# Kernel tuning notes

Measured on AMD Instinct MI355X. Metric: run time of the kernel, lower is better.

Reference implementation:

```python
import jax, jax.numpy as jnp
import numpy as np

B, S, H = 32, 512, 768
N, E, P = 4096, 131072, 65536
HEADS1, C1 = 4, 128
HEADS2, C2 = 1, 64
NUM_REL, REL_HID = 6, 256
NER_HID, NER_LAB = 256, 9
LRELU_SLOPE = 0.2  # PyG GATConv default negative_slope
LN_EPS = 1e-5


def setup_inputs() -> dict:
    key = jax.random.key(0)
    ks = jax.random.split(key, 24)
    sc = 0.02
    inp = {
        'sequence_output': jax.random.normal(ks[0], (B, S, H), jnp.float32),
        'ent_start': jax.random.randint(ks[1], (N,), 0, S - 8),
        'ent_len': jax.random.randint(ks[2], (N,), 0, 8),
        'ent_batch': jax.random.randint(ks[3], (N,), 0, B),
        'edge_index': jax.random.randint(ks[4], (2, E), 0, N),
        'pair_idx': jax.random.randint(ks[5], (P, 2), 0, N),
        'W1': jax.random.normal(ks[6], (H, HEADS1 * C1), jnp.float32) * sc,
        'a_src1': jax.random.normal(ks[7], (HEADS1, C1), jnp.float32) * sc,
        'a_dst1': jax.random.normal(ks[8], (HEADS1, C1), jnp.float32) * sc,
        'b1': jnp.zeros((HEADS1 * C1,), jnp.float32),
        'W2': jax.random.normal(ks[9], (HEADS1 * C1, HEADS2 * C2), jnp.float32) * sc,
        'a_src2': jax.random.normal(ks[10], (HEADS2, C2), jnp.float32) * sc,
        'a_dst2': jax.random.normal(ks[11], (HEADS2, C2), jnp.float32) * sc,
        'b2': jnp.zeros((HEADS2 * C2,), jnp.float32),
        # 6 per-relation classifiers: Linear(128,256)+LN+ReLU+Linear(256,1)
        'relW1': jax.random.normal(ks[12], (NUM_REL, 2 * C2, REL_HID), jnp.float32) * sc,
        'relb1': jnp.zeros((NUM_REL, REL_HID), jnp.float32),
        'ln_g': jnp.ones((NUM_REL, REL_HID), jnp.float32),
        'ln_b': jnp.zeros((NUM_REL, REL_HID), jnp.float32),
        'relW2': jax.random.normal(ks[13], (NUM_REL, REL_HID, 1), jnp.float32) * sc,
        'relb2': jnp.zeros((NUM_REL, 1), jnp.float32),
        # NER head: Linear(768,256)+ReLU+Linear(256,9)
        'nerW1': jax.random.normal(ks[14], (H, NER_HID), jnp.float32) * sc,
        'nerb1': jnp.zeros((NER_HID,), jnp.float32),
        'nerW2': jax.random.normal(ks[15], (NER_HID, NER_LAB), jnp.float32) * sc,
        'nerb2': jnp.zeros((NER_LAB,), jnp.float32),
    }
    return inp


def _gat(x, src, dst, W, a_src, a_dst, b, heads, ch, n):
    # PyG GATConv: per-head linear, additive attention, softmax over incoming edges
    h = (x @ W).reshape(n, heads, ch)                      # [N,Hd,C]
    e_src = jnp.sum(h * a_src, axis=-1)                    # [N,Hd]
    e_dst = jnp.sum(h * a_dst, axis=-1)
    e = jax.nn.leaky_relu(e_src[src] + e_dst[dst], LRELU_SLOPE)  # [E,Hd]
    m = jax.ops.segment_max(e, dst, num_segments=n)
    ex = jnp.exp(e - m[dst])
    denom = jax.ops.segment_sum(ex, dst, num_segments=n)
    alpha = ex / denom[dst]                                # [E,Hd]
    out = jax.ops.segment_sum(alpha[:, :, None] * h[src], dst, num_segments=n)
    return out.reshape(n, heads * ch) + b


def reference(sequence_output, ent_start, ent_len, ent_batch, edge_index, pair_idx,
              W1, a_src1, a_dst1, b1, W2, a_src2, a_dst2, b2,
              relW1, relb1, ln_g, ln_b, relW2, relb2,
              nerW1, nerb1, nerW2, nerb2):
    n = ent_start.shape[0]
    # NER head on the full sequence
    ner_logits = jax.nn.relu(sequence_output @ nerW1 + nerb1) @ nerW2 + nerb2  # [B,S,9]
    # Entity-span mean pooling via exclusive prefix sums (inclusive span start..start+len)
    csum = jnp.cumsum(sequence_output, axis=1)
    csum = jnp.concatenate([jnp.zeros((B, 1, H), sequence_output.dtype), csum], axis=1)  # [B,S+1,H]
    ent_end = ent_start + ent_len
    span_sum = csum[ent_batch, ent_end + 1] - csum[ent_batch, ent_start]  # [N,H]
    x = span_sum / (ent_len + 1).astype(span_sum.dtype)[:, None]
    # add self loops (PyG GATConv default add_self_loops=True)
    loops = jnp.arange(n, dtype=edge_index.dtype)
    src = jnp.concatenate([edge_index[0], loops])
    dst = jnp.concatenate([edge_index[1], loops])
    x = _gat(x, src, dst, W1, a_src1, a_dst1, b1, HEADS1, C1, n)
    x = jax.nn.relu(x)  # dropout p=0.3 is identity in eval mode
    x = _gat(x, src, dst, W2, a_src2, a_dst2, b2, HEADS2, C2, n)  # [N,64]
    # Pair features: cat(x[e1], x[e2]) -> [P,128]
    pair_feat = jnp.concatenate([x[pair_idx[:, 0]], x[pair_idx[:, 1]]], axis=-1)
    # All 6 relation classifiers, vectorized over the relation dim
    hid = jnp.einsum('pf,rfk->rpk', pair_feat, relW1) + relb1[:, None, :]  # [6,P,256]
    mu = jnp.mean(hid, axis=-1, keepdims=True)
    var = jnp.mean(jnp.square(hid - mu), axis=-1, keepdims=True)
    hid = (hid - mu) * jax.lax.rsqrt(var + LN_EPS) * ln_g[:, None, :] + ln_b[:, None, :]
    hid = jax.nn.relu(hid)
    rel_logits = (jnp.einsum('rpk,rko->rpo', hid, relW2) + relb2[:, None, :])[..., 0]  # [6,P]
    return ner_logits, rel_logits
```

## Files before the change

kernel.cpp:

```cpp
#include <hip/hip_runtime.h>
#include <math.h>

#define LRELU 0.2f

constexpr int Bn = 32, Sn = 512, Hn = 768, Nn = 4096, En = 131072, Pn = 65536;
constexpr int ET = En + Nn;

typedef __attribute__((ext_vector_type(8))) short bf16x8;
typedef __attribute__((ext_vector_type(4))) float f32x4;

constexpr size_t OFF_X0  = 0;
constexpr size_t OFF_UV  = 0;
constexpr size_t OFF_H1  = 4194304;
constexpr size_t OFF_X1  = OFF_H1  + 2097152;
constexpr size_t OFF_H2  = OFF_X1  + 2097152;
constexpr size_t OFF_X2  = OFF_H2  + 262144;
constexpr size_t OFF_ES1 = OFF_X2  + 262144;
constexpr size_t OFF_ED1 = OFF_ES1 + 16384;
constexpr size_t OFF_ES2 = OFF_ED1 + 16384;
constexpr size_t OFF_ED2 = OFF_ES2 + 4096;
constexpr size_t OFF_ROW = OFF_ED2 + 4096;
constexpr size_t OFF_CUR = OFF_ROW + 4104;
constexpr size_t OFF_EDG = OFF_CUR + 4096;
constexpr size_t OFF_W1S = OFF_EDG + 135168;
constexpr size_t OFF_NW1S = OFF_W1S + 196608;

__device__ __forceinline__ short f2bf(float f) {
  union { float f; unsigned u; } x; x.f = f;
  unsigned r = x.u + 0x7fff + ((x.u >> 16) & 1);
  return (short)(r >> 16);
}
__device__ __forceinline__ float bf2f(short s) {
  union { unsigned u; float f; } x;
  x.u = ((unsigned)(unsigned short)s) << 16;
  return x.f;
}

__global__ __launch_bounds__(256) void span_pool_k(
    const float* __restrict__ seq, const int* __restrict__ est,
    const int* __restrict__ eln, const int* __restrict__ ebt,
    float* __restrict__ x0) {
  int idx = blockIdx.x * 256 + threadIdx.x;
  if (idx >= Nn * (Hn / 4)) return;
  int e = idx / (Hn / 4);
  int c = (idx % (Hn / 4)) * 4;
  int s0 = est[e], L = eln[e] + 1, b = ebt[e];
  const float* p = seq + ((size_t)b * Sn + s0) * Hn + c;
  float ax = 0, ay = 0, az = 0, aw = 0;
  for (int i = 0; i < L; ++i) {
    float4 v = *(const float4*)(p + (size_t)i * Hn);
    ax += v.x; ay += v.y; az += v.z; aw += v.w;
  }
  float inv = 1.0f / (float)L;
  float4 o; o.x = ax * inv; o.y = ay * inv; o.z = az * inv; o.w = aw * inv;
  *(float4*)&x0[(size_t)e * Hn + c] = o;
}

template <int EPI, int NTW, int KC>
__global__ __launch_bounds__(256) void mfma_gemm_k(
    const float* __restrict__ A, const short* __restrict__ Bswz,
    float* __restrict__ C, const float* __restrict__ bias,
    int M, int K, int N) {
  constexpr int RS = KC + 8;
  __shared__ short at[64 * RS];
  int t = threadIdx.x;
  size_t rowb = (size_t)blockIdx.x * 64;
  int colb = blockIdx.y * (64 * NTW);
  int w = t >> 6, lane = t & 63, quad = lane >> 4, id = lane & 15;
  f32x4 acc[4][NTW];
#pragma unroll
  for (int mt = 0; mt < 4; ++mt)
#pragma unroll
    for (int nt = 0; nt < NTW; ++nt) acc[mt][nt] = (f32x4){0.f, 0.f, 0.f, 0.f};

  for (int k0 = 0; k0 < K; k0 += KC) {
    constexpr int CH = 64 * KC / 8 / 256;
#pragma unroll
    for (int i = 0; i < CH; ++i) {
      int cid = t + i * 256;
      int p = cid / (KC / 8), o8 = (cid % (KC / 8)) * 8;
      const float* src = &A[(rowb + p) * (size_t)K + k0 + o8];
      float4 v0 = *(const float4*)src;
      float4 v1 = *(const float4*)(src + 4);
      bf16x8 bv;
      bv[0] = f2bf(v0.x); bv[1] = f2bf(v0.y); bv[2] = f2bf(v0.z); bv[3] = f2bf(v0.w);
      bv[4] = f2bf(v1.x); bv[5] = f2bf(v1.y); bv[6] = f2bf(v1.z); bv[7] = f2bf(v1.w);
      *(bf16x8*)&at[p * RS + o8] = bv;
    }
    __syncthreads();
#pragma unroll
    for (int kk = 0; kk < KC / 32; ++kk) {
      bf16x8 af[4], bfr[NTW];
#pragma unroll
      for (int mt = 0; mt < 4; ++mt)
        af[mt] = *(const bf16x8*)&at[(mt * 16 + id) * RS + kk * 32 + quad * 8];
#pragma unroll
      for (int nt = 0; nt < NTW; ++nt) {
        int ntg = (colb >> 4) + w * NTW + nt;
        bfr[nt] = *(const bf16x8*)&Bswz[(((size_t)(k0 >> 5) + kk) * (N >> 4) + ntg) * 512 + lane * 8];
      }
#pragma unroll
      for (int mt = 0; mt < 4; ++mt)
#pragma unroll
        for (int nt = 0; nt < NTW; ++nt)
          acc[mt][nt] = __builtin_amdgcn_mfma_f32_16x16x32_bf16(af[mt], bfr[nt], acc[mt][nt], 0, 0, 0);
    }
    __syncthreads();
  }
#pragma unroll
  for (int nt = 0; nt < NTW; ++nt) {
    int col = colb + w * (16 * NTW) + nt * 16 + id;
#pragma unroll
    for (int mt = 0; mt < 4; ++mt) {
#pragma unroll
      for (int reg = 0; reg < 4; ++reg) {
        size_t row = rowb + mt * 16 + quad * 4 + reg;
        float v = acc[mt][nt][reg];
        if (EPI == 2) ((short*)C)[row * (size_t)N + col] = f2bf(v);
        else          C[row * (size_t)N + col] = v;
      }
    }
  }
}

__global__ __launch_bounds__(256) void ner_fused_k(
    const float* __restrict__ A, const short* __restrict__ Bswz,
    const float* __restrict__ W2, const float* __restrict__ b1,
    const float* __restrict__ b2, float* __restrict__ out) {
  constexpr int K = 768, N = 256;
  constexpr int RS = 136, HS = 264, WS = 260;
  __shared__ short at[64 * RS];
  __shared__ short hid[64 * HS];
  __shared__ float w2t[9 * WS];
  __shared__ float b2l[9];
  int t = threadIdx.x;
  size_t rowb = (size_t)blockIdx.x * 64;
  for (int u = t; u < 2304; u += 256) {
    int k = u / 9, jj = u % 9;
    w2t[jj * WS + k] = W2[u];
  }
  if (t < 9) b2l[t] = b2[t];
  int w = t >> 6, lane = t & 63, quad = lane >> 4, id = lane & 15;
  f32x4 acc[4][4];
#pragma unroll
  for (int mt = 0; mt < 4; ++mt)
#pragma unroll
    for (int nt = 0; nt < 4; ++nt) acc[mt][nt] = (f32x4){0.f, 0.f, 0.f, 0.f};

  for (int k0 = 0; k0 < K; k0 += 128) {
#pragma unroll
    for (int i = 0; i < 4; ++i) {
      int cid = t + i * 256;
      int p = cid >> 4, o8 = (cid & 15) * 8;
      const float* src = &A[(rowb + p) * (size_t)K + k0 + o8];
      float4 v0 = *(const float4*)src;
      float4 v1 = *(const float4*)(src + 4);
      bf16x8 bv;
      bv[0] = f2bf(v0.x); bv[1] = f2bf(v0.y); bv[2] = f2bf(v0.z); bv[3] = f2bf(v0.w);
      bv[4] = f2bf(v1.x); bv[5] = f2bf(v1.y); bv[6] = f2bf(v1.z); bv[7] = f2bf(v1.w);
      *(bf16x8*)&at[p * RS + o8] = bv;
    }
    __syncthreads();
#pragma unroll
    for (int kk = 0; kk < 4; ++kk) {
      bf16x8 af[4], bfr[4];
#pragma unroll
      for (int mt = 0; mt < 4; ++mt)
        af[mt] = *(const bf16x8*)&at[(mt * 16 + id) * RS + kk * 32 + quad * 8];
#pragma unroll
      for (int nt = 0; nt < 4; ++nt) {
        int ntg = w * 4 + nt;
        bfr[nt] = *(const bf16x8*)&Bswz[(((size_t)(k0 >> 5) + kk) * 16 + ntg) * 512 + lane * 8];
      }
#pragma unroll
      for (int mt = 0; mt < 4; ++mt)
#pragma unroll
        for (int nt = 0; nt < 4; ++nt)
          acc[mt][nt] = __builtin_amdgcn_mfma_f32_16x16x32_bf16(af[mt], bfr[nt], acc[mt][nt], 0, 0, 0);
    }
    __syncthreads();
  }
#pragma unroll
  for (int nt = 0; nt < 4; ++nt) {
    int col = w * 64 + nt * 16 + id;
    float bb = b1[col];
#pragma unroll
    for (int mt = 0; mt < 4; ++mt)
#pragma unroll
      for (int reg = 0; reg < 4; ++reg) {
        int row = mt * 16 + quad * 4 + reg;
        hid[row * HS + col] = f2bf(fmaxf(acc[mt][nt][reg] + bb, 0.f));
      }
  }
  __syncthreads();
  for (int u = t; u < 576; u += 256) {
    int row = u / 9, jj = u % 9;
    const short* hp = &hid[row * HS];
    const float* wp = &w2t[jj * WS];
    float a = 0.f;
#pragma unroll
    for (int k8 = 0; k8 < 256; k8 += 8) {
      bf16x8 hv = *(const bf16x8*)&hp[k8];
      float4 w0 = *(const float4*)&wp[k8];
      float4 w1 = *(const float4*)&wp[k8 + 4];
      a += bf2f(hv[0]) * w0.x + bf2f(hv[1]) * w0.y + bf2f(hv[2]) * w0.z + bf2f(hv[3]) * w0.w;
      a += bf2f(hv[4]) * w1.x + bf2f(hv[5]) * w1.y + bf2f(hv[6]) * w1.z + bf2f(hv[7]) * w1.w;
    }
    out[(rowb + row) * 9 + jj] = a + b2l[jj];
  }
}

template <int K, int N>
__global__ void swz_k(const float* __restrict__ B, short* __restrict__ o) {
  int i = blockIdx.x * 256 + threadIdx.x;
  if (i >= K * N) return;
  int n = i % N, k = i / N;
  int kk = k >> 5, quad = (k >> 3) & 3, j = k & 7, ntg = n >> 4, id = n & 15;
  o[(((size_t)kk * (N >> 4)) + ntg) * 512 + (quad * 16 + id) * 8 + j] = f2bf(B[i]);
}

__global__ void swz_uv_k(const float* __restrict__ rW1, short* __restrict__ o) {
  int i = blockIdx.x * 256 + threadIdx.x;
  if (i >= 6 * 128 * 256) return;
  int n = i & 255, k = (i >> 8) & 127, r = i >> 15;
  int c = r * 512 + (k >> 6) * 256 + n;
  int kr = k & 63;
  int kk = kr >> 5, quad = (kr >> 3) & 3, j = kr & 7, ntg = c >> 4, id = c & 15;
  o[(((size_t)kk * 192) + ntg) * 512 + (quad * 16 + id) * 8 + j] = f2bf(rW1[i]);
}

template <int HD, int C>
__global__ __launch_bounds__(256) void coef_k(
    const float* __restrict__ h, const float* __restrict__ a_src,
    const float* __restrict__ a_dst, float* __restrict__ es, float* __restrict__ ed) {
  int idx = blockIdx.x * 256 + threadIdx.x;
  if (idx >= Nn * HD) return;
  int n = idx / HD, hd = idx % HD;
  const float* hp = h + (size_t)n * HD * C + hd * C;
  const float* sp = a_src + hd * C;
  const float* dp = a_dst + hd * C;
  float s = 0, d = 0;
  for (int c = 0; c < C; c += 4) {
    float4 v = *(const float4*)(hp + c);
    float4 a = *(const float4*)(sp + c);
    float4 b = *(const float4*)(dp + c);
    s += v.x * a.x + v.y * a.y + v.z * a.z + v.w * a.w;
    d += v.x * b.x + v.y * b.y + v.z * b.z + v.w * b.w;
  }
  es[idx] = s; ed[idx] = d;
}

__global__ void zero_k(int* __restrict__ p, int n) {
  int i = blockIdx.x * 256 + threadIdx.x;
  if (i < n) p[i] = 0;
}

__global__ void count_k(const int* __restrict__ eidx, int* __restrict__ cnt) {
  int i = blockIdx.x * 256 + threadIdx.x;
  if (i >= ET) return;
  int dst = (i < En) ? eidx[En + i] : (i - En);
  atomicAdd(&cnt[dst], 1);
}

__global__ __launch_bounds__(256) void scan_k(int* cnt_cur, int* rowoff) {
  __shared__ int s[256];
  int t = threadIdx.x;
  int loc[16]; int run = 0; int base = t * 16;
#pragma unroll
  for (int i = 0; i < 16; ++i) { loc[i] = run; run += cnt_cur[base + i]; }
  s[t] = run;
  __syncthreads();
  for (int off = 1; off < 256; off <<= 1) {
    int v = (t >= off) ? s[t - off] : 0;
    __syncthreads();
    s[t] += v;
    __syncthreads();
  }
  int offset = (t > 0) ? s[t - 1] : 0;
#pragma unroll
  for (int i = 0; i < 16; ++i) {
    int o = offset + loc[i];
    rowoff[base + i] = o;
    cnt_cur[base + i] = o;
  }
  if (t == 255) rowoff[4096] = s[255];
}

__global__ void scatter_k(const int* __restrict__ eidx, int* __restrict__ cur,
                          int* __restrict__ esrc) {
  int i = blockIdx.x * 256 + threadIdx.x;
  if (i >= ET) return;
  int s, d;
  if (i < En) { s = eidx[i]; d = eidx[En + i]; } else { s = d = i - En; }
  int pos = atomicAdd(&cur[d], 1);
  esrc[pos] = s;
}

__global__ void pcount_k(const int* __restrict__ pidx, int* __restrict__ cnt) {
  int p = blockIdx.x * 256 + threadIdx.x;
  if (p < Pn) atomicAdd(&cnt[pidx[2 * p]], 1);
}

__global__ void pscatter_k(const int* __restrict__ pidx, int* __restrict__ cur,
                           int2* __restrict__ plist) {
  int p = blockIdx.x * 256 + threadIdx.x;
  if (p >= Pn) return;
  int i = pidx[2 * p];
  int pos = atomicAdd(&cur[i], 1);
  plist[pos] = make_int2(pidx[2 * p + 1], p);
}

template <int HD, int C, bool RELU>
__global__ __launch_bounds__(256) void gat_agg_k(
    const float* __restrict__ h, const float* __restrict__ es,
    const float* __restrict__ ed, const int* __restrict__ row_off,
    const int* __restrict__ eslist, const float* __restrict__ bias,
    float* __restrict__ xout) {
  constexpr int CAP = 320;
  __shared__ float red[256];
  __shared__ float mxs[HD], dns[HD];
  __shared__ float exc[CAP * HD];
  int n = blockIdx.x, t = threadIdx.x;
  int ro = row_off[n], deg = row_off[n + 1] - ro;
  int hd = t % HD, ei = t / HD;
  constexpr int ES = 256 / HD;
  float edv = ed[n * HD + hd];
  float pm = -3.402823466e38f;
  for (int j = ei; j < deg; j += ES) {
    int s = eslist[ro + j];
    float e = es[s * HD + hd] + edv;
    e = (e > 0.f) ? e : LRELU * e;
    pm = fmaxf(pm, e);
  }
  red[t] = pm;
  __syncthreads();
  for (int off = 128; off >= HD; off >>= 1) {
    if (t < off) red[t] = fmaxf(red[t], red[t + off]);
    __syncthreads();
  }
  if (t < HD) mxs[t] = red[t];
  __syncthreads();
  float mx = mxs[hd];
  float ps = 0.f;
  for (int j = ei; j < deg; j += ES) {
    int s = eslist[ro + j];
    float e = es[s * HD + hd] + edv;
    e = (e > 0.f) ? e : LRELU * e;
    float ex = __expf(e - mx);
    if (j < CAP) exc[j * HD + hd] = ex;
    ps += ex;
  }
  red[t] = ps;
  __syncthreads();
  for (int off = 128; off >= HD; off >>= 1) {
    if (t < off) red[t] += red[t + off];
    __syncthreads();
  }
  if (t < HD) dns[t] = red[t];
  __syncthreads();
  for (int c = t; c < HD * C; c += 256) {
    int hh = c / C;
    float mxh = mxs[hh], edh = ed[n * HD + hh];
    float acc = 0.f;
    for (int j = 0; j < deg; ++j) {
      int s = eslist[ro + j];
      float ex;
      if (j < CAP) ex = exc[j * HD + hh];
      else {
        float e = es[s * HD + hh] + edh;
        e = (e > 0.f) ? e : LRELU * e;
        ex = __expf(e - mxh);
      }
      acc += ex * h[(size_t)s * (HD * C) + c];
    }
    float v = acc / dns[hh] + bias[c];
    if (RELU) v = fmaxf(v, 0.f);
    xout[(size_t)n * (HD * C) + c] = v;
  }
}

__global__ __launch_bounds__(256) void pair_rel2_k(
    const short* __restrict__ UV, const int* __restrict__ prow,
    const int2* __restrict__ plist, const float* __restrict__ rb1,
    const float* __restrict__ lng, const float* __restrict__ lnb,
    const float* __restrict__ rW2, const float* __restrict__ rb2,
    float* __restrict__ out) {
  int t = threadIdx.x;
  int r = blockIdx.y;
  int w = t >> 6, lane = t & 63;
  int pg = lane >> 4, l16 = lane & 15;
  int n = blockIdx.x * 4 + w;
  int cb = r * 256 + l16 * 16;
  float rbl[16], g[16], bb[16], wv[16];
#pragma unroll
  for (int q = 0; q < 4; ++q) {
    *(float4*)&rbl[q * 4] = *(const float4*)&rb1[cb + q * 4];
    *(float4*)&g[q * 4]   = *(const float4*)&lng[cb + q * 4];
    *(float4*)&bb[q * 4]  = *(const float4*)&lnb[cb + q * 4];
    *(float4*)&wv[q * 4]  = *(const float4*)&rW2[cb + q * 4];
  }
  float rb2v = rb2[r];
  const short* up = &UV[(size_t)n * 3072 + r * 512 + l16 * 16];
  bf16x8 u0 = *(const bf16x8*)up, u1 = *(const bf16x8*)(up + 8);
  float ur[16];
#pragma unroll
  for (int cc = 0; cc < 8; ++cc) {
    ur[cc] = bf2f(u0[cc]) + rbl[cc];
    ur[8 + cc] = bf2f(u1[cc]) + rbl[8 + cc];
  }
  int ro = prow[n], deg = prow[n + 1] - ro;
  for (int base = 0; base < deg; base += 4) {
    int slot = base + pg;
    bool act = slot < deg;
    int2 jp = act ? plist[ro + slot] : make_int2(0, 0);
    const short* vp = &UV[(size_t)jp.x * 3072 + r * 512 + 256 + l16 * 16];
    bf16x8 v0 = *(const bf16x8*)vp, v1 = *(const bf16x8*)(vp + 8);
    float hv[16], s1 = 0.f, s2 = 0.f;
#pragma unroll
    for (int cc = 0; cc < 8; ++cc) {
      float h = ur[cc] + bf2f(v0[cc]);
      hv[cc] = h; s1 += h; s2 += h * h;
    }
#pragma unroll
    for (int cc = 0; cc < 8; ++cc) {
      float h = ur[8 + cc] + bf2f(v1[cc]);
      hv[8 + cc] = h; s1 += h; s2 += h * h;
    }
#pragma unroll
    for (int off = 1; off < 16; off <<= 1) {
      s1 += __shfl_xor(s1, off, 64);
      s2 += __shfl_xor(s2, off, 64);
    }
    float mu = s1 * (1.f / 256.f);
    float var = s2 * (1.f / 256.f) - mu * mu;
    float rs = rsqrtf(var + 1e-5f);
    float pv = 0.f;
#pragma unroll
    for (int cc = 0; cc < 16; ++cc) {
      float v = (hv[cc] - mu) * rs * g[cc] + bb[cc];
      v = fmaxf(v, 0.f);
      pv += v * wv[cc];
    }
#pragma unroll
    for (int off = 1; off < 16; off <<= 1) pv += __shfl_xor(pv, off, 64);
    if (l16 == 0 && act) out[(size_t)r * Pn + jp.y] = pv + rb2v;
  }
}

extern "C" void kernel_launch(void* const* d_in, const int* in_sizes, int n_in,
                              void* d_out, int out_size, void* d_ws, size_t ws_size,
                              hipStream_t stream) {
  const float* seq = (const float*)d_in[0];
  const int* est = (const int*)d_in[1];
  const int* eln = (const int*)d_in[2];
  const int* ebt = (const int*)d_in[3];
  const int* eidx = (const int*)d_in[4];
  const int* pidx = (const int*)d_in[5];
  const float* W1 = (const float*)d_in[6];
  const float* as1 = (const float*)d_in[7];
  const float* ad1 = (const float*)d_in[8];
  const float* b1 = (const float*)d_in[9];
  const float* W2 = (const float*)d_in[10];
  const float* as2 = (const float*)d_in[11];
  const float* ad2 = (const float*)d_in[12];
  const float* b2 = (const float*)d_in[13];
  const float* rW1 = (const float*)d_in[14];
  const float* rb1 = (const float*)d_in[15];
  const float* lng = (const float*)d_in[16];
  const float* lnb = (const float*)d_in[17];
  const float* rW2 = (const float*)d_in[18];
  const float* rb2 = (const float*)d_in[19];
  const float* nW1 = (const float*)d_in[20];
  const float* nb1 = (const float*)d_in[21];
  const float* nW2 = (const float*)d_in[22];
  const float* nb2 = (const float*)d_in[23];
  float* out = (float*)d_out;
  float* ws = (float*)d_ws;

  float* x0 = ws + OFF_X0;
  short* uv = (short*)(ws + OFF_UV);
  float* h1 = ws + OFF_H1;
  float* x1 = ws + OFF_X1;
  float* h2 = ws + OFF_H2;
  short* uvw = (short*)(ws + OFF_H2);
  float* x2 = ws + OFF_X2;
  float* es1 = ws + OFF_ES1;
  float* ed1 = ws + OFF_ED1;
  float* es2 = ws + OFF_ES2;
  float* ed2 = ws + OFF_ED2;
  int* rowoff = (int*)(ws + OFF_ROW);
  int* cur = (int*)(ws + OFF_CUR);
  int* edg = (int*)(ws + OFF_EDG);
  short* w1s = (short*)(ws + OFF_W1S);
  short* w2s = (short*)(ws + OFF_W1S);
  short* nw1s = (short*)(ws + OFF_NW1S);
  int* prow = (int*)(ws + OFF_X1);
  int* pcur = (int*)(ws + OFF_X1 + 4104);
  int2* plist = (int2*)(ws + OFF_X1 + 8208);

  zero_k<<<16, 256, 0, stream>>>(cur, Nn);
  count_k<<<(ET + 255) / 256, 256, 0, stream>>>(eidx, cur);
  scan_k<<<1, 256, 0, stream>>>(cur, rowoff);
  scatter_k<<<(ET + 255) / 256, 256, 0, stream>>>(eidx, cur, edg);
  swz_k<768, 512><<<(768 * 512 + 255) / 256, 256, 0, stream>>>(W1, w1s);
  swz_k<768, 256><<<(768 * 256 + 255) / 256, 256, 0, stream>>>(nW1, nw1s);

  span_pool_k<<<Nn * (Hn / 4) / 256, 256, 0, stream>>>(seq, est, eln, ebt, x0);

  mfma_gemm_k<0, 2, 128><<<dim3(Nn / 64, 512 / 128), 256, 0, stream>>>(x0, w1s, h1, nullptr, Nn, Hn, 512);
  swz_k<512, 64><<<(512 * 64 + 255) / 256, 256, 0, stream>>>(W2, w2s);
  coef_k<4, 128><<<(Nn * 4) / 256, 256, 0, stream>>>(h1, as1, ad1, es1, ed1);
  gat_agg_k<4, 128, true><<<Nn, 256, 0, stream>>>(h1, es1, ed1, rowoff, edg, b1, x1);

  mfma_gemm_k<0, 1, 128><<<dim3(Nn / 64, 1), 256, 0, stream>>>(x1, w2s, h2, nullptr, Nn, 512, 64);

  zero_k<<<16, 256, 0, stream>>>(pcur, Nn);
  pcount_k<<<Pn / 256, 256, 0, stream>>>(pidx, pcur);
  scan_k<<<1, 256, 0, stream>>>(pcur, prow);
  pscatter_k<<<Pn / 256, 256, 0, stream>>>(pidx, pcur, plist);

  coef_k<1, 64><<<(Nn + 255) / 256, 256, 0, stream>>>(h2, as2, ad2, es2, ed2);
  gat_agg_k<1, 64, false><<<Nn, 256, 0, stream>>>(h2, es2, ed2, rowoff, edg, b2, x2);

  swz_uv_k<<<(6 * 128 * 256) / 256, 256, 0, stream>>>(rW1, uvw);
  mfma_gemm_k<2, 2, 64><<<dim3(Nn / 64, 3072 / 128), 256, 0, stream>>>(x2, uvw, (float*)uv, nullptr, Nn, 64, 3072);
  pair_rel2_k<<<dim3(Nn / 4, 6), 256, 0, stream>>>(uv, prow, plist, rb1, lng, lnb, rW2, rb2,
                                                   out + (size_t)Bn * Sn * 9);

  ner_fused_k<<<(Bn * Sn) / 64, 256, 0, stream>>>(seq, nw1s, nW2, nb1, nb2, out);
}
```

Before: 395.6 us.

## Store GAT projections in bf16, vectorize aggregation, drop pair CSR sort

```diff
diff --git a/kernel.cpp b/kernel.cpp
--- a/kernel.cpp
+++ b/kernel.cpp
@@ -127,7 +127,7 @@
     const float* __restrict__ A, const short* __restrict__ Bswz,
     const float* __restrict__ W2, const float* __restrict__ b1,
     const float* __restrict__ b2, float* __restrict__ out) {
-  constexpr int K = 768, N = 256;
+  constexpr int K = 768;
   constexpr int RS = 136, HS = 264, WS = 260;
   __shared__ short at[64 * RS];
   __shared__ short hid[64 * HS];
@@ -230,22 +230,24 @@
 }
 
 template <int HD, int C>
-__global__ __launch_bounds__(256) void coef_k(
-    const float* __restrict__ h, const float* __restrict__ a_src,
+__global__ __launch_bounds__(256) void coef_b_k(
+    const short* __restrict__ h, const float* __restrict__ a_src,
     const float* __restrict__ a_dst, float* __restrict__ es, float* __restrict__ ed) {
   int idx = blockIdx.x * 256 + threadIdx.x;
   if (idx >= Nn * HD) return;
   int n = idx / HD, hd = idx % HD;
-  const float* hp = h + (size_t)n * HD * C + hd * C;
+  const short* hp = h + (size_t)n * HD * C + hd * C;
   const float* sp = a_src + hd * C;
   const float* dp = a_dst + hd * C;
   float s = 0, d = 0;
-  for (int c = 0; c < C; c += 4) {
-    float4 v = *(const float4*)(hp + c);
-    float4 a = *(const float4*)(sp + c);
-    float4 b = *(const float4*)(dp + c);
-    s += v.x * a.x + v.y * a.y + v.z * a.z + v.w * a.w;
-    d += v.x * b.x + v.y * b.y + v.z * b.z + v.w * b.w;
+  for (int c = 0; c < C; c += 8) {
+    bf16x8 v = *(const bf16x8*)(hp + c);
+#pragma unroll
+    for (int k = 0; k < 8; ++k) {
+      float f = bf2f(v[k]);
+      s += f * sp[c + k];
+      d += f * dp[c + k];
+    }
   }
   es[idx] = s; ed[idx] = d;
 }
@@ -296,30 +298,18 @@
   esrc[pos] = s;
 }
 
-__global__ void pcount_k(const int* __restrict__ pidx, int* __restrict__ cnt) {
-  int p = blockIdx.x * 256 + threadIdx.x;
-  if (p < Pn) atomicAdd(&cnt[pidx[2 * p]], 1);
-}
-
-__global__ void pscatter_k(const int* __restrict__ pidx, int* __restrict__ cur,
-                           int2* __restrict__ plist) {
-  int p = blockIdx.x * 256 + threadIdx.x;
-  if (p >= Pn) return;
-  int i = pidx[2 * p];
-  int pos = atomicAdd(&cur[i], 1);
-  plist[pos] = make_int2(pidx[2 * p + 1], p);
-}
-
 template <int HD, int C, bool RELU>
 __global__ __launch_bounds__(256) void gat_agg_k(
-    const float* __restrict__ h, const float* __restrict__ es,
+    const short* __restrict__ h, const float* __restrict__ es,
     const float* __restrict__ ed, const int* __restrict__ row_off,
     const int* __restrict__ eslist, const float* __restrict__ bias,
     float* __restrict__ xout) {
+  constexpr int HDC = HD * C, OCT = HDC / 8, JS = 256 / OCT;
   constexpr int CAP = 320;
   __shared__ float red[256];
   __shared__ float mxs[HD], dns[HD];
   __shared__ float exc[CAP * HD];
+  __shared__ float part[JS * HDC];
   int n = blockIdx.x, t = threadIdx.x;
   int ro = row_off[n], deg = row_off[n + 1] - ro;
   int hd = t % HD, ei = t / HD;
@@ -358,40 +348,50 @@
   }
   if (t < HD) dns[t] = red[t];
   __syncthreads();
-  for (int c = t; c < HD * C; c += 256) {
-    int hh = c / C;
-    float mxh = mxs[hh], edh = ed[n * HD + hh];
-    float acc = 0.f;
-    for (int j = 0; j < deg; ++j) {
-      int s = eslist[ro + j];
-      float ex;
-      if (j < CAP) ex = exc[j * HD + hh];
-      else {
-        float e = es[s * HD + hh] + edh;
-        e = (e > 0.f) ? e : LRELU * e;
-        ex = __expf(e - mxh);
-      }
-      acc += ex * h[(size_t)s * (HD * C) + c];
-    }
-    float v = acc / dns[hh] + bias[c];
+  int oc = t % OCT, js = t / OCT;
+  int hh = oc / (C / 8);
+  float mxh = mxs[hh], edh = ed[n * HD + hh];
+  float a[8];
+#pragma unroll
+  for (int k = 0; k < 8; ++k) a[k] = 0.f;
+  for (int j = js; j < deg; j += JS) {
+    int s = eslist[ro + j];
+    float ex;
+    if (j < CAP) ex = exc[j * HD + hh];
+    else {
+      float e = es[s * HD + hh] + edh;
+      e = (e > 0.f) ? e : LRELU * e;
+      ex = __expf(e - mxh);
+    }
+    bf16x8 hv = *(const bf16x8*)&h[(size_t)s * HDC + oc * 8];
+#pragma unroll
+    for (int k = 0; k < 8; ++k) a[k] += ex * bf2f(hv[k]);
+  }
+#pragma unroll
+  for (int k = 0; k < 8; ++k) part[js * HDC + oc * 8 + k] = a[k];
+  __syncthreads();
+  for (int c = t; c < HDC; c += 256) {
+    float sum = 0.f;
+#pragma unroll
+    for (int q = 0; q < JS; ++q) sum += part[q * HDC + c];
+    int hh2 = c / C;
+    float v = sum / dns[hh2] + bias[c];
     if (RELU) v = fmaxf(v, 0.f);
-    xout[(size_t)n * (HD * C) + c] = v;
-  }
-}
-
-__global__ __launch_bounds__(256) void pair_rel2_k(
-    const short* __restrict__ UV, const int* __restrict__ prow,
-    const int2* __restrict__ plist, const float* __restrict__ rb1,
-    const float* __restrict__ lng, const float* __restrict__ lnb,
-    const float* __restrict__ rW2, const float* __restrict__ rb2,
-    float* __restrict__ out) {
+    xout[(size_t)n * HDC + c] = v;
+  }
+}
+
+__global__ __launch_bounds__(256) void pair_rel_k(
+    const short* __restrict__ UV, const int* __restrict__ pidx,
+    const float* __restrict__ rb1, const float* __restrict__ lng,
+    const float* __restrict__ lnb, const float* __restrict__ rW2,
+    const float* __restrict__ rb2, float* __restrict__ out) {
   int t = threadIdx.x;
   int r = blockIdx.y;
   int w = t >> 6, lane = t & 63;
   int pg = lane >> 4, l16 = lane & 15;
-  int n = blockIdx.x * 4 + w;
+  float rbl[16], g[16], bb[16], wv[16];
   int cb = r * 256 + l16 * 16;
-  float rbl[16], g[16], bb[16], wv[16];
 #pragma unroll
   for (int q = 0; q < 4; ++q) {
     *(float4*)&rbl[q * 4] = *(const float4*)&rb1[cb + q * 4];
@@ -400,30 +400,23 @@
     *(float4*)&wv[q * 4]  = *(const float4*)&rW2[cb + q * 4];
   }
   float rb2v = rb2[r];
-  const short* up = &UV[(size_t)n * 3072 + r * 512 + l16 * 16];
-  bf16x8 u0 = *(const bf16x8*)up, u1 = *(const bf16x8*)(up + 8);
-  float ur[16];
-#pragma unroll
-  for (int cc = 0; cc < 8; ++cc) {
-    ur[cc] = bf2f(u0[cc]) + rbl[cc];
-    ur[8 + cc] = bf2f(u1[cc]) + rbl[8 + cc];
-  }
-  int ro = prow[n], deg = prow[n + 1] - ro;
-  for (int base = 0; base < deg; base += 4) {
-    int slot = base + pg;
-    bool act = slot < deg;
-    int2 jp = act ? plist[ro + slot] : make_int2(0, 0);
-    const short* vp = &UV[(size_t)jp.x * 3072 + r * 512 + 256 + l16 * 16];
+  int pbase = blockIdx.x * 256 + w * 64;
+  for (int it = 0; it < 16; ++it) {
+    int p = pbase + it * 4 + pg;
+    int i = pidx[p * 2], j = pidx[p * 2 + 1];
+    const short* up = &UV[(size_t)i * 3072 + r * 512 + l16 * 16];
+    const short* vp = &UV[(size_t)j * 3072 + r * 512 + 256 + l16 * 16];
+    bf16x8 u0 = *(const bf16x8*)up, u1 = *(const bf16x8*)(up + 8);
     bf16x8 v0 = *(const bf16x8*)vp, v1 = *(const bf16x8*)(vp + 8);
     float hv[16], s1 = 0.f, s2 = 0.f;
 #pragma unroll
     for (int cc = 0; cc < 8; ++cc) {
-      float h = ur[cc] + bf2f(v0[cc]);
+      float h = bf2f(u0[cc]) + bf2f(v0[cc]) + rbl[cc];
       hv[cc] = h; s1 += h; s2 += h * h;
     }
 #pragma unroll
     for (int cc = 0; cc < 8; ++cc) {
-      float h = ur[8 + cc] + bf2f(v1[cc]);
+      float h = bf2f(u1[cc]) + bf2f(v1[cc]) + rbl[8 + cc];
       hv[8 + cc] = h; s1 += h; s2 += h * h;
     }
 #pragma unroll
@@ -443,7 +436,7 @@
     }
 #pragma unroll
     for (int off = 1; off < 16; off <<= 1) pv += __shfl_xor(pv, off, 64);
-    if (l16 == 0 && act) out[(size_t)r * Pn + jp.y] = pv + rb2v;
+    if (l16 == 0) out[(size_t)r * Pn + p] = pv + rb2v;
   }
 }
 
@@ -479,9 +472,9 @@
 
   float* x0 = ws + OFF_X0;
   short* uv = (short*)(ws + OFF_UV);
-  float* h1 = ws + OFF_H1;
+  short* h1 = (short*)(ws + OFF_H1);
   float* x1 = ws + OFF_X1;
-  float* h2 = ws + OFF_H2;
+  short* h2 = (short*)(ws + OFF_H2);
   short* uvw = (short*)(ws + OFF_H2);
   float* x2 = ws + OFF_X2;
   float* es1 = ws + OFF_ES1;
@@ -494,9 +487,6 @@
   short* w1s = (short*)(ws + OFF_W1S);
   short* w2s = (short*)(ws + OFF_W1S);
   short* nw1s = (short*)(ws + OFF_NW1S);
-  int* prow = (int*)(ws + OFF_X1);
-  int* pcur = (int*)(ws + OFF_X1 + 4104);
-  int2* plist = (int2*)(ws + OFF_X1 + 8208);
 
   zero_k<<<16, 256, 0, stream>>>(cur, Nn);
   count_k<<<(ET + 255) / 256, 256, 0, stream>>>(eidx, cur);
@@ -507,25 +497,19 @@
 
   span_pool_k<<<Nn * (Hn / 4) / 256, 256, 0, stream>>>(seq, est, eln, ebt, x0);
 
-  mfma_gemm_k<0, 2, 128><<<dim3(Nn / 64, 512 / 128), 256, 0, stream>>>(x0, w1s, h1, nullptr, Nn, Hn, 512);
+  mfma_gemm_k<2, 2, 128><<<dim3(Nn / 64, 512 / 128), 256, 0, stream>>>(x0, w1s, (float*)h1, nullptr, Nn, Hn, 512);
   swz_k<512, 64><<<(512 * 64 + 255) / 256, 256, 0, stream>>>(W2, w2s);
-  coef_k<4, 128><<<(Nn * 4) / 256, 256, 0, stream>>>(h1, as1, ad1, es1, ed1);
+  coef_b_k<4, 128><<<(Nn * 4) / 256, 256, 0, stream>>>(h1, as1, ad1, es1, ed1);
   gat_agg_k<4, 128, true><<<Nn, 256, 0, stream>>>(h1, es1, ed1, rowoff, edg, b1, x1);
 
-  mfma_gemm_k<0, 1, 128><<<dim3(Nn / 64, 1), 256, 0, stream>>>(x1, w2s, h2, nullptr, Nn, 512, 64);
-
-  zero_k<<<16, 256, 0, stream>>>(pcur, Nn);
-  pcount_k<<<Pn / 256, 256, 0, stream>>>(pidx, pcur);
-  scan_k<<<1, 256, 0, stream>>>(pcur, prow);
-  pscatter_k<<<Pn / 256, 256, 0, stream>>>(pidx, pcur, plist);
-
-  coef_k<1, 64><<<(Nn + 255) / 256, 256, 0, stream>>>(h2, as2, ad2, es2, ed2);
+  mfma_gemm_k<2, 1, 128><<<dim3(Nn / 64, 1), 256, 0, stream>>>(x1, w2s, (float*)h2, nullptr, Nn, 512, 64);
+  coef_b_k<1, 64><<<(Nn + 255) / 256, 256, 0, stream>>>(h2, as2, ad2, es2, ed2);
   gat_agg_k<1, 64, false><<<Nn, 256, 0, stream>>>(h2, es2, ed2, rowoff, edg, b2, x2);
 
   swz_uv_k<<<(6 * 128 * 256) / 256, 256, 0, stream>>>(rW1, uvw);
   mfma_gemm_k<2, 2, 64><<<dim3(Nn / 64, 3072 / 128), 256, 0, stream>>>(x2, uvw, (float*)uv, nullptr, Nn, 64, 3072);
-  pair_rel2_k<<<dim3(Nn / 4, 6), 256, 0, stream>>>(uv, prow, plist, rb1, lng, lnb, rW2, rb2,
-                                                   out + (size_t)Bn * Sn * 9);
+  pair_rel_k<<<dim3(Pn / 256, 6), 256, 0, stream>>>(uv, pidx, rb1, lng, lnb, rW2, rb2,
+                                                    out + (size_t)Bn * Sn * 9);
 
   ner_fused_k<<<(Bn * Sn) / 64, 256, 0, stream>>>(seq, nw1s, nW2, nb1, nb2, out);
 }
```

Result: faster. 342.1 us (-13.5%).
